# Kernel optimization log

Measured on AMD Instinct MI355X. Metric: run time of the kernel, lower is better.

## Reference

```python
import jax, jax.numpy as jnp
import numpy as np
from functools import partial

MAX_INSTANCES = 8


def _conv(x, W, b):
    y = jax.lax.conv_general_dilated(x, W, (1, 1), 'SAME',
                                     dimension_numbers=('NHWC', 'HWIO', 'NHWC'))
    return jax.nn.relu(y + b)


def _conv_stack(x, params):
    for W, b in params:
        x = _conv(x, W, b)
    return x


def _resize_and_pad(feat, info, bg_h, bg_w):
    # feat: (h, w, c); info: [y1, y2, x1, x2] fractions of bg size.
    # Bilinear resize (half-pixel centers, like tf.image.resize) of feat to
    # (y_size, x_size), then zero-pad into the (bg_h, bg_w) canvas at
    # (y_front, x_front). Expressed as a fixed-shape gather + validity mask
    # so it is jit-compatible despite data-dependent box sizes.
    h, w, _ = feat.shape
    y_size = jnp.maximum((bg_h * (info[1] - info[0])).astype(jnp.int32), 1)
    x_size = jnp.maximum((bg_w * (info[3] - info[2])).astype(jnp.int32), 1)
    y_front = (bg_h * info[0]).astype(jnp.int32)
    x_front = (bg_w * info[2]).astype(jnp.int32)

    def axis(bg_n, front, size, n_in):
        loc = jnp.arange(bg_n) - front
        valid = (loc >= 0) & (loc < size)
        src = (loc.astype(jnp.float32) + 0.5) * (n_in / size.astype(jnp.float32)) - 0.5
        src = jnp.clip(src, 0.0, n_in - 1.0)
        i0 = jnp.floor(src).astype(jnp.int32)
        i1 = jnp.minimum(i0 + 1, n_in - 1)
        return i0, i1, src - i0.astype(jnp.float32), valid

    y0, y1i, fy, vy = axis(bg_h, y_front, y_size, h)
    x0, x1i, fx, vx = axis(bg_w, x_front, x_size, w)
    g = lambda yi, xi: feat[yi][:, xi]  # (bg_h, bg_w, c)
    fy = fy[:, None, None]
    fx = fx[None, :, None]
    out = (g(y0, x0) * (1 - fy) * (1 - fx) + g(y0, x1i) * (1 - fy) * fx
           + g(y1i, x0) * fy * (1 - fx) + g(y1i, x1i) * fy * fx)
    return out * (vy[:, None] & vx[None, :]).astype(feat.dtype)[:, :, None]


def setup_inputs() -> dict:
    key = jax.random.key(0)
    ks = jax.random.split(key, 16)
    B, H, W, C = 4, 128, 128, 64
    h = w = 64
    hm = wm = 56
    U = 64
    MI = MAX_INSTANCES
    instance_feature = jax.random.normal(ks[0], (B, h, w, C, MI), jnp.float32)
    bg_feature = jax.random.normal(ks[1], (B, H, W, C), jnp.float32)
    # Valid boxes: 0 <= y1 < y2 <= 1, 0 <= x1 < x2 <= 1, layout (B, 4, MI).
    y1 = jax.random.uniform(ks[2], (B, 1, MI), minval=0.0, maxval=0.45)
    hh = jax.random.uniform(ks[3], (B, 1, MI), minval=0.2, maxval=0.5)
    x1 = jax.random.uniform(ks[4], (B, 1, MI), minval=0.0, maxval=0.45)
    ww = jax.random.uniform(ks[5], (B, 1, MI), minval=0.2, maxval=0.5)
    bbox = jnp.concatenate([y1, y1 + hh, x1, x1 + ww], axis=1)
    mrcnn_mask = jax.random.uniform(ks[6], (B, hm, wm, MI), jnp.float32)
    s = 0.05  # small weights keep exp() of relu conv outputs well-scaled
    return {
        'instance_feature': instance_feature,
        'bg_feature': bg_feature,
        'bbox': bbox,
        'mrcnn_mask': mrcnn_mask,
        'iW1': jax.random.normal(ks[7], (3, 3, C, U), jnp.float32) * s,
        'ib1': jnp.zeros((U,), jnp.float32),
        'iW2': jax.random.normal(ks[8], (3, 3, U, U), jnp.float32) * s,
        'ib2': jnp.zeros((U,), jnp.float32),
        'iW3': jax.random.normal(ks[9], (3, 3, U, 1), jnp.float32) * s,
        'ib3': jnp.zeros((1,), jnp.float32),
        'bW1': jax.random.normal(ks[10], (3, 3, C, U), jnp.float32) * s,
        'bb1': jnp.zeros((U,), jnp.float32),
        'bW2': jax.random.normal(ks[11], (3, 3, U, U), jnp.float32) * s,
        'bb2': jnp.zeros((U,), jnp.float32),
        'bW3': jax.random.normal(ks[12], (3, 3, U, 1), jnp.float32) * s,
        'bb3': jnp.zeros((1,), jnp.float32),
    }


def reference(instance_feature, bg_feature, bbox, mrcnn_mask,
              iW1, ib1, iW2, ib2, iW3, ib3,
              bW1, bb1, bW2, bb2, bW3, bb3):
    B, H, W, C = bg_feature.shape
    MI = instance_feature.shape[-1]
    h, w = instance_feature.shape[1], instance_feature.shape[2]
    # pack_instance -> conv stack -> unpack (kept as (B, MI, h, w, 1))
    packed = jnp.transpose(instance_feature, (0, 4, 1, 2, 3)).reshape(B * MI, h, w, C)
    iw = _conv_stack(packed, [(iW1, ib1), (iW2, ib2), (iW3, ib3)]).reshape(B, MI, h, w, 1)
    bgw = _conv_stack(bg_feature, [(bW1, bb1), (bW2, bb2), (bW3, bb3)])  # (B,H,W,1)

    rp = jax.vmap(jax.vmap(partial(_resize_and_pad, bg_h=H, bg_w=W)))
    bbox_t = jnp.transpose(bbox, (0, 2, 1))  # (B, MI, 4)
    rw = rp(iw, bbox_t)  # (B, MI, H, W, 1)
    full = jnp.broadcast_to(jnp.array([0.0, 1.0, 0.0, 1.0], jnp.float32), (B, MI, 4))
    rm = rp(jnp.moveaxis(mrcnn_mask, -1, 1)[..., None], full)  # (B, MI, H, W, 1)
    rsf = rp(jnp.moveaxis(instance_feature, -1, 1), bbox_t)  # (B, MI, H, W, C)

    ew = jnp.exp(rw) * rm          # per-instance exp weight, masked
    ew_bg = jnp.exp(bgw)           # (B, H, W, 1)
    denom = ew.sum(axis=1) + ew_bg  # (B, H, W, 1)
    return (ew_bg / denom) * bg_feature + jnp.sum(rsf * (ew / denom[:, None]), axis=1)
```

## Files before the change

### kernel.cpp

```cpp
#include <hip/hip_runtime.h>
#include <cstdint>

typedef short bf16x8 __attribute__((ext_vector_type(8)));
typedef float f32x4 __attribute__((ext_vector_type(4)));
typedef unsigned short u16;
typedef unsigned short u16x8 __attribute__((ext_vector_type(8)));
typedef unsigned int u32;

__device__ inline u16 f2bf(float f) {
  union { float f; unsigned u; } x; x.f = f;
  unsigned u = x.u + 0x7fffu + ((x.u >> 16) & 1u);
  return (u16)(u >> 16);
}
__device__ inline float bf2f(u16 h) {
  union { unsigned u; float f; } x; x.u = ((unsigned)h) << 16;
  return x.f;
}

__global__ __launch_bounds__(256) void transpose_inst(
    const float* __restrict__ inst, u16* __restrict__ pf)
{
  const int lane = threadIdx.x & 63;
  const int wvid = blockIdx.x * 4 + (threadIdx.x >> 6);
  const int b = wvid >> 12;
  const int pix = wvid & 4095;
  const float* s = inst + ((size_t)(b * 4096 + pix)) * 512 + lane * 8;
  float4 v0 = *(const float4*)s;
  float4 v1 = *(const float4*)(s + 4);
  float vals[8] = {v0.x, v0.y, v0.z, v0.w, v1.x, v1.y, v1.z, v1.w};
  #pragma unroll
  for (int i = 0; i < 8; i++)
    pf[(((size_t)(b * 8 + i)) * 4096 + pix) * 64 + lane] = f2bf(vals[i]);
}

__global__ __launch_bounds__(256) void wtrans(
    const float* __restrict__ w0, const float* __restrict__ w1,
    const float* __restrict__ w2, const float* __restrict__ w3,
    u16* __restrict__ wtr)
{
  int id = blockIdx.x * 256 + threadIdx.x;
  if (id >= 147456) return;
  int s = id / 36864;
  int r = id - s * 36864;
  int tap = r >> 12;
  int rc = r & 4095;
  int c = rc >> 6, u = rc & 63;
  const float* Ws = (s == 0) ? w0 : (s == 1) ? w1 : (s == 2) ? w2 : w3;
  wtr[(size_t)s * 36864 + ((size_t)tap * 64 + u) * 64 + c] =
      f2bf(Ws[((size_t)tap * 64 + c) * 64 + u]);
}

#define BOFF 41472
template<int SRC>
__device__ __forceinline__ void conv_body(
    char* smem, const void* __restrict__ inv, const u16* __restrict__ wtr,
    const float* __restrict__ bias, u16* __restrict__ out,
    int H, int W, int bid)
{
  const int tilesX = W >> 4;
  const int tilesPerImg = (H >> 4) * tilesX;
  const int img = bid / tilesPerImg;
  const int tile = bid - img * tilesPerImg;
  const int ty = (tile / tilesX) << 4;
  const int tx = (tile % tilesX) << 4;
  const int tid = threadIdx.x;

  for (int idx = tid; idx < 2592; idx += 256) {
    int hpix = idx >> 3;
    int c0 = (idx & 7) << 3;
    int hy = hpix / 18, hx = hpix - hy * 18;
    int gy = ty + hy - 1, gx = tx + hx - 1;
    u16x8 v = {0, 0, 0, 0, 0, 0, 0, 0};
    if (gy >= 0 && gy < H && gx >= 0 && gx < W) {
      if (SRC == 0) {
        const float* s = (const float*)inv + ((size_t)img * H * W + (size_t)gy * W + gx) * 64 + c0;
        #pragma unroll
        for (int j = 0; j < 8; j++) v[j] = f2bf(s[j]);
      } else if (SRC == 1) {
        const u16* s = (const u16*)inv + ((size_t)img * H * W + (size_t)gy * W + gx) * 64 + c0;
        v = *(const u16x8*)s;
      } else {
        int bb = img >> 3, ii = img & 7;
        const float* s = (const float*)inv + ((((size_t)bb * 64 + gy) * 64 + gx) * 64 + c0) * 8 + ii;
        #pragma unroll
        for (int j = 0; j < 8; j++) v[j] = f2bf(s[j * 8]);
      }
    }
    int byte = (hpix * 128 + c0 * 2) ^ ((hpix & 7) << 4);
    *(u16x8*)(smem + byte) = v;
  }

  const int lane = tid & 63;
  const int wv = tid >> 6;
  const int lrow = lane & 15;
  const int kg = lane >> 4;

  const int ch0 = tid, ch1 = tid + 256;
  const int bu0 = ch0 >> 3, bc0 = (ch0 & 7) << 3;
  const int bu1 = ch1 >> 3, bc1 = (ch1 & 7) << 3;
  const int bdst0 = BOFF + ((bu0 * 128 + bc0 * 2) ^ ((bu0 & 7) << 4));
  const int bdst1 = BOFF + ((bu1 * 128 + bc1 * 2) ^ ((bu1 & 7) << 4));

  {
    u16x8 n0 = *(const u16x8*)(wtr + (size_t)(0 * 64 + bu0) * 64 + bc0);
    u16x8 n1 = *(const u16x8*)(wtr + (size_t)(0 * 64 + bu1) * 64 + bc1);
    *(u16x8*)(smem + bdst0) = n0;
    *(u16x8*)(smem + bdst1) = n1;
  }
  __syncthreads();

  int pyv[4], pxv[4];
  #pragma unroll
  for (int mf = 0; mf < 4; mf++) {
    int p = wv * 64 + mf * 16 + lrow;
    pyv[mf] = p >> 4; pxv[mf] = p & 15;
  }

  f32x4 acc[4][4];
  #pragma unroll
  for (int a = 0; a < 4; a++)
    #pragma unroll
    for (int b = 0; b < 4; b++) { f32x4 z = {0.f, 0.f, 0.f, 0.f}; acc[a][b] = z; }

  for (int tap = 0; tap < 9; tap++) {
    u16x8 n0, n1;
    if (tap < 8) {
      n0 = *(const u16x8*)(wtr + (size_t)((tap + 1) * 64 + bu0) * 64 + bc0);
      n1 = *(const u16x8*)(wtr + (size_t)((tap + 1) * 64 + bu1) * 64 + bc1);
    }
    const int ky = tap / 3, kx = tap - ky * 3;
    #pragma unroll
    for (int ks = 0; ks < 2; ks++) {
      bf16x8 Bf[4];
      #pragma unroll
      for (int nf = 0; nf < 4; nf++) {
        int u = nf * 16 + lrow;
        int byte = BOFF + ((u * 128 + ks * 64 + kg * 16) ^ ((u & 7) << 4));
        Bf[nf] = *(const bf16x8*)(smem + byte);
      }
      #pragma unroll
      for (int mf = 0; mf < 4; mf++) {
        int hpix = (pyv[mf] + ky) * 18 + pxv[mf] + kx;
        int byte = (hpix * 128 + ks * 64 + kg * 16) ^ ((hpix & 7) << 4);
        bf16x8 Af = *(const bf16x8*)(smem + byte);
        #pragma unroll
        for (int nf = 0; nf < 4; nf++)
          acc[mf][nf] = __builtin_amdgcn_mfma_f32_16x16x32_bf16(Af, Bf[nf], acc[mf][nf], 0, 0, 0);
      }
    }
    __syncthreads();
    if (tap < 8) {
      *(u16x8*)(smem + bdst0) = n0;
      *(u16x8*)(smem + bdst1) = n1;
      __syncthreads();
    }
  }

  float bv[4];
  #pragma unroll
  for (int nf = 0; nf < 4; nf++) bv[nf] = bias[nf * 16 + lrow];

  const size_t obase = (size_t)img * H * W;
  #pragma unroll
  for (int mf = 0; mf < 4; mf++) {
    #pragma unroll
    for (int j = 0; j < 4; j++) {
      int p = wv * 64 + mf * 16 + kg * 4 + j;
      int oy = ty + (p >> 4), ox = tx + (p & 15);
      u16* op = out + (obase + (size_t)oy * W + ox) * 64 + lrow;
      #pragma unroll
      for (int nf = 0; nf < 4; nf++)
        op[nf * 16] = f2bf(fmaxf(acc[mf][nf][j] + bv[nf], 0.0f));
    }
  }
}

template<int S1, int S2>
__global__ __launch_bounds__(256) void conv_dual(
    const void* in1, const u16* w1, const float* b1, u16* o1, int H1, int W1, int split,
    const void* in2, const u16* w2, const float* b2, u16* o2, int H2, int W2)
{
  extern __shared__ float4 smem_f4[];
  char* smem = (char*)smem_f4;
  if ((int)blockIdx.x < split)
    conv_body<S1>(smem, in1, w1, b1, o1, H1, W1, blockIdx.x);
  else
    conv_body<S2>(smem, in2, w2, b2, o2, H2, W2, blockIdx.x - split);
}

__device__ __forceinline__ void conv3_body(
    char* smem, const u16* __restrict__ in, const float* __restrict__ W3,
    const float* __restrict__ b3, float* __restrict__ out, int H, int W, int bid)
{
  float* wlds = (float*)(smem + 41472);
  const int tilesX = W >> 4;
  const int tilesPerImg = (H >> 4) * tilesX;
  const int img = bid / tilesPerImg;
  const int tile = bid - img * tilesPerImg;
  const int ty = (tile / tilesX) << 4;
  const int tx = (tile % tilesX) << 4;
  const int tid = threadIdx.x;

  for (int idx = tid; idx < 2592; idx += 256) {
    int hpix = idx >> 3;
    int c0 = (idx & 7) << 3;
    int hy = hpix / 18, hx = hpix - hy * 18;
    int gy = ty + hy - 1, gx = tx + hx - 1;
    u16x8 v = {0, 0, 0, 0, 0, 0, 0, 0};
    if (gy >= 0 && gy < H && gx >= 0 && gx < W)
      v = *(const u16x8*)(in + ((size_t)img * H * W + (size_t)gy * W + gx) * 64 + c0);
    int byte = (hpix * 128 + c0 * 2) ^ ((hpix & 7) << 4);
    *(u16x8*)(smem + byte) = v;
  }
  for (int idx = tid; idx < 576; idx += 256) wlds[idx] = W3[idx];
  __syncthreads();

  const int py = tid >> 4, px = tid & 15;
  float acc = 0.0f;
  #pragma unroll
  for (int ky = 0; ky < 3; ky++) {
    #pragma unroll
    for (int kx = 0; kx < 3; kx++) {
      const int hpix = (py + ky) * 18 + (px + kx);
      const float* wp = wlds + (ky * 3 + kx) * 64;
      #pragma unroll
      for (int cg = 0; cg < 8; cg++) {
        int byte = (hpix * 128 + cg * 16) ^ ((hpix & 7) << 4);
        u16x8 v = *(const u16x8*)(smem + byte);
        #pragma unroll
        for (int j = 0; j < 8; j++)
          acc = fmaf(bf2f(v[j]), wp[cg * 8 + j], acc);
      }
    }
  }
  out[(size_t)img * H * W + (size_t)(ty + py) * W + (tx + px)] =
      fmaxf(acc + b3[0], 0.0f);
}

__global__ __launch_bounds__(256) void conv3_dual(
    const u16* in1, const float* W31, const float* b31, float* o1, int H1, int W1, int split,
    const u16* in2, const float* W32, const float* b32, float* o2, int H2, int W2)
{
  extern __shared__ float4 smem_f4[];
  char* smem = (char*)smem_f4;
  if ((int)blockIdx.x < split)
    conv3_body(smem, in1, W31, b31, o1, H1, W1, blockIdx.x);
  else
    conv3_body(smem, in2, W32, b32, o2, H2, W2, blockIdx.x - split);
}

__global__ __launch_bounds__(256) void precompute_params(
    const float* __restrict__ bbox, const float* __restrict__ mask,
    const float* __restrict__ iw, const float* __restrict__ bgw,
    float* __restrict__ pp_wbg, float* __restrict__ pp_wi,
    u32* __restrict__ pp_yx, float* __restrict__ pp_fy, float* __restrict__ pp_fx)
{
  const int gpix = blockIdx.x * 256 + threadIdx.x;
  const int b = gpix >> 14;
  const int p = gpix & 16383;
  const int Y = p >> 7, X = p & 127;

  float msy = ((float)Y + 0.5f) * 0.4375f - 0.5f;
  msy = fminf(fmaxf(msy, 0.0f), 55.0f);
  int my0 = (int)floorf(msy); int my1 = min(my0 + 1, 55); float fmy = msy - (float)my0;
  float msx = ((float)X + 0.5f) * 0.4375f - 0.5f;
  msx = fminf(fmaxf(msx, 0.0f), 55.0f);
  int mx0 = (int)floorf(msx); int mx1 = min(mx0 + 1, 55); float fmx = msx - (float)mx0;

  const float ewbg = expf(bgw[gpix]);
  float denom = ewbg;
  float wi_l[8];
  u32 yx_l[8];
  float fy_l[8], fx_l[8];

  #pragma unroll
  for (int i = 0; i < 8; i++) {
    float by1 = bbox[(b * 4 + 0) * 8 + i];
    float by2 = bbox[(b * 4 + 1) * 8 + i];
    float bx1 = bbox[(b * 4 + 2) * 8 + i];
    float bx2 = bbox[(b * 4 + 3) * 8 + i];
    int ysz = max((int)(128.0f * (by2 - by1)), 1);
    int xsz = max((int)(128.0f * (bx2 - bx1)), 1);
    int yfr = (int)(128.0f * by1);
    int xfr = (int)(128.0f * bx1);
    int ly = Y - yfr, lx = X - xfr;
    bool valid = (ly >= 0) && (ly < ysz) && (lx >= 0) && (lx < xsz);
    float rwv = 0.0f;
    int y0 = 0, y1i = 0, x0 = 0, x1i = 0;
    float fy = 0.0f, fx = 0.0f;
    if (valid) {
      float sy = ((float)ly + 0.5f) * (64.0f / (float)ysz) - 0.5f;
      sy = fminf(fmaxf(sy, 0.0f), 63.0f);
      y0 = (int)floorf(sy); y1i = min(y0 + 1, 63); fy = sy - (float)y0;
      float sx = ((float)lx + 0.5f) * (64.0f / (float)xsz) - 0.5f;
      sx = fminf(fmaxf(sx, 0.0f), 63.0f);
      x0 = (int)floorf(sx); x1i = min(x0 + 1, 63); fx = sx - (float)x0;
      const float* iwp = iw + ((size_t)(b * 8 + i)) * 4096;
      float v00 = iwp[y0 * 64 + x0],  v01 = iwp[y0 * 64 + x1i];
      float v10 = iwp[y1i * 64 + x0], v11 = iwp[y1i * 64 + x1i];
      rwv = v00 * (1.f - fy) * (1.f - fx) + v01 * (1.f - fy) * fx
          + v10 * fy * (1.f - fx)         + v11 * fy * fx;
    }
    const float* mp = mask + (size_t)b * 56 * 56 * 8 + i;
    float m00 = mp[(my0 * 56 + mx0) * 8], m01 = mp[(my0 * 56 + mx1) * 8];
    float m10 = mp[(my1 * 56 + mx0) * 8], m11 = mp[(my1 * 56 + mx1) * 8];
    float rm = m00 * (1.f - fmy) * (1.f - fmx) + m01 * (1.f - fmy) * fmx
             + m10 * fmy * (1.f - fmx)         + m11 * fmy * fmx;
    float ew = expf(rwv) * rm;
    denom += ew;
    wi_l[i] = valid ? ew : 0.0f;
    yx_l[i] = (u32)y0 | ((u32)x0 << 8) | ((u32)y1i << 16) | ((u32)x1i << 24);
    fy_l[i] = fy; fx_l[i] = fx;
  }

  const float invd = 1.0f / denom;
  pp_wbg[gpix] = ewbg * invd;
  #pragma unroll
  for (int i = 0; i < 8; i++) {
    pp_wi[i * 65536 + gpix] = wi_l[i] * invd;
    pp_yx[i * 65536 + gpix] = yx_l[i];
    pp_fy[i * 65536 + gpix] = fy_l[i];
    pp_fx[i * 65536 + gpix] = fx_l[i];
  }
}

__global__ __launch_bounds__(256) void final_blend(
    const u16* __restrict__ pf, const float* __restrict__ bgf,
    const float* __restrict__ pp_wbg, const float* __restrict__ pp_wi,
    const u32* __restrict__ pp_yx, const float* __restrict__ pp_fy,
    const float* __restrict__ pp_fx, float* __restrict__ out)
{
  const int lane = threadIdx.x & 63;
  const int gpix = blockIdx.x * 4 + (threadIdx.x >> 6);
  const int b = gpix >> 14;

  float accv = pp_wbg[gpix] * bgf[(size_t)gpix * 64 + lane];
  #pragma unroll
  for (int i = 0; i < 8; i++) {
    float wiv = pp_wi[i * 65536 + gpix];
    if (wiv != 0.0f) {
      u32 yx = pp_yx[i * 65536 + gpix];
      float fy = pp_fy[i * 65536 + gpix];
      float fx = pp_fx[i * 65536 + gpix];
      int y0 = yx & 255, x0 = (yx >> 8) & 255;
      int y1i = (yx >> 16) & 255, x1i = (yx >> 24) & 255;
      const u16* fp = pf + (size_t)(b * 8 + i) * 262144;
      float g00 = bf2f(fp[((size_t)(y0 * 64 + x0)) * 64 + lane]);
      float g01 = bf2f(fp[((size_t)(y0 * 64 + x1i)) * 64 + lane]);
      float g10 = bf2f(fp[((size_t)(y1i * 64 + x0)) * 64 + lane]);
      float g11 = bf2f(fp[((size_t)(y1i * 64 + x1i)) * 64 + lane]);
      float s = g00 * (1.f - fy) * (1.f - fx) + g01 * (1.f - fy) * fx
              + g10 * fy * (1.f - fx)         + g11 * fy * fx;
      accv = fmaf(wiv, s, accv);
    }
  }
  out[(size_t)gpix * 64 + lane] = accv;
}

__global__ __launch_bounds__(256) void final_kernel_fb(
    const float* __restrict__ inst, const float* __restrict__ bgf,
    const float* __restrict__ bbox, const float* __restrict__ mask,
    const float* __restrict__ iw, const float* __restrict__ bgw,
    float* __restrict__ out)
{
  const int lane = threadIdx.x & 63;
  const int wvid = blockIdx.x * 4 + (threadIdx.x >> 6);
  const int nw = gridDim.x * 4;
  for (int pix = wvid; pix < 4 * 128 * 128; pix += nw) {
    const int b = pix >> 14;
    const int p = pix & 16383;
    const int Y = p >> 7, X = p & 127;

    float msy = ((float)Y + 0.5f) * 0.4375f - 0.5f;
    msy = fminf(fmaxf(msy, 0.0f), 55.0f);
    int my0 = (int)floorf(msy); int my1 = min(my0 + 1, 55); float fmy = msy - (float)my0;
    float msx = ((float)X + 0.5f) * 0.4375f - 0.5f;
    msx = fminf(fmaxf(msx, 0.0f), 55.0f);
    int mx0 = (int)floorf(msx); int mx1 = min(mx0 + 1, 55); float fmx = msx - (float)mx0;

    const float ewbg = expf(bgw[(size_t)b * 16384 + p]);
    float denom = ewbg;
    float acc = 0.0f;

    for (int i = 0; i < 8; i++) {
      float by1 = bbox[(b * 4 + 0) * 8 + i];
      float by2 = bbox[(b * 4 + 1) * 8 + i];
      float bx1 = bbox[(b * 4 + 2) * 8 + i];
      float bx2 = bbox[(b * 4 + 3) * 8 + i];
      int ysz = max((int)(128.0f * (by2 - by1)), 1);
      int xsz = max((int)(128.0f * (bx2 - bx1)), 1);
      int yfr = (int)(128.0f * by1);
      int xfr = (int)(128.0f * bx1);
      int ly = Y - yfr, lx = X - xfr;
      bool valid = (ly >= 0) && (ly < ysz) && (lx >= 0) && (lx < xsz);
      float rwv = 0.0f;
      int y0 = 0, y1i = 0, x0 = 0, x1i = 0;
      float fy = 0.0f, fx = 0.0f;
      if (valid) {
        float sy = ((float)ly + 0.5f) * (64.0f / (float)ysz) - 0.5f;
        sy = fminf(fmaxf(sy, 0.0f), 63.0f);
        y0 = (int)floorf(sy); y1i = min(y0 + 1, 63); fy = sy - (float)y0;
        float sx = ((float)lx + 0.5f) * (64.0f / (float)xsz) - 0.5f;
        sx = fminf(fmaxf(sx, 0.0f), 63.0f);
        x0 = (int)floorf(sx); x1i = min(x0 + 1, 63); fx = sx - (float)x0;
        const float* iwp = iw + ((size_t)(b * 8 + i)) * 4096;
        float v00 = iwp[y0 * 64 + x0],  v01 = iwp[y0 * 64 + x1i];
        float v10 = iwp[y1i * 64 + x0], v11 = iwp[y1i * 64 + x1i];
        rwv = v00 * (1.f - fy) * (1.f - fx) + v01 * (1.f - fy) * fx
            + v10 * fy * (1.f - fx)         + v11 * fy * fx;
      }
      const float* mp = mask + (size_t)b * 56 * 56 * 8 + i;
      float m00 = mp[(my0 * 56 + mx0) * 8], m01 = mp[(my0 * 56 + mx1) * 8];
      float m10 = mp[(my1 * 56 + mx0) * 8], m11 = mp[(my1 * 56 + mx1) * 8];
      float rm = m00 * (1.f - fmy) * (1.f - fmx) + m01 * (1.f - fmy) * fmx
               + m10 * fmy * (1.f - fmx)         + m11 * fmy * fmx;
      float ew = expf(rwv) * rm;
      denom += ew;
      if (valid) {
        const float* fp = inst + (size_t)b * 2097152 + i;
        float g00 = fp[(((size_t)y0 * 64 + x0) * 64 + lane) * 8];
        float g01 = fp[(((size_t)y0 * 64 + x1i) * 64 + lane) * 8];
        float g10 = fp[(((size_t)y1i * 64 + x0) * 64 + lane) * 8];
        float g11 = fp[(((size_t)y1i * 64 + x1i) * 64 + lane) * 8];
        float s = g00 * (1.f - fy) * (1.f - fx) + g01 * (1.f - fy) * fx
                + g10 * fy * (1.f - fx)         + g11 * fy * fx;
        acc += ew * s;
      }
    }
    const float bgv = bgf[((size_t)b * 16384 + p) * 64 + lane];
    out[((size_t)b * 16384 + p) * 64 + lane] = (ewbg * bgv + acc) / denom;
  }
}

extern "C" void kernel_launch(void* const* d_in, const int* in_sizes, int n_in,
                              void* d_out, int out_size, void* d_ws, size_t ws_size,
                              hipStream_t stream) {
  const float* inst = (const float*)d_in[0];
  const float* bgf  = (const float*)d_in[1];
  const float* bbox = (const float*)d_in[2];
  const float* mask = (const float*)d_in[3];
  const float* iW1 = (const float*)d_in[4];  const float* ib1 = (const float*)d_in[5];
  const float* iW2 = (const float*)d_in[6];  const float* ib2 = (const float*)d_in[7];
  const float* iW3 = (const float*)d_in[8];  const float* ib3 = (const float*)d_in[9];
  const float* bW1 = (const float*)d_in[10]; const float* bb1 = (const float*)d_in[11];
  const float* bW2 = (const float*)d_in[12]; const float* bb2 = (const float*)d_in[13];
  const float* bW3 = (const float*)d_in[14]; const float* bb3 = (const float*)d_in[15];

  char* ws = (char*)d_ws;
  u16*   wtr  = (u16*)ws;
  u16*   AbI  = (u16*)(ws + 294912);
  u16*   AbB  = (u16*)(ws + 17072128);
  u16*   BbI  = (u16*)(ws + 25460736);
  u16*   BbB  = (u16*)(ws + 42237952);
  float* iw   = (float*)(ws + 50626560);
  float* bgw  = (float*)(ws + 51150848);
  u16*   pf   = (u16*)(ws + 51412992);
  const bool usePf = ws_size >= (size_t)68190208;
  float* outp = (float*)d_out;

  float* pp_wbg = (float*)(ws + 294912);
  float* pp_wi  = (float*)(ws + 294912 + 262144);
  u32*   pp_yx  = (u32*)  (ws + 294912 + 2359296);
  float* pp_fy  = (float*)(ws + 294912 + 4456448);
  float* pp_fx  = (float*)(ws + 294912 + 6553600);

  wtrans<<<576, 256, 0, stream>>>(iW1, iW2, bW1, bW2, wtr);

  if (usePf) {
    transpose_inst<<<4096, 256, 0, stream>>>(inst, pf);
    conv_dual<1, 0><<<768, 256, 49664, stream>>>(
        pf,  wtr,             ib1, AbI, 64, 64, 512,
        bgf, wtr + 2 * 36864, bb1, AbB, 128, 128);
    conv_dual<1, 1><<<768, 256, 49664, stream>>>(
        AbI, wtr + 36864,     ib2, BbI, 64, 64, 512,
        AbB, wtr + 3 * 36864, bb2, BbB, 128, 128);
    conv3_dual<<<768, 256, 43776, stream>>>(
        BbI, iW3, ib3, iw, 64, 64, 512,
        BbB, bW3, bb3, bgw, 128, 128);
    precompute_params<<<256, 256, 0, stream>>>(bbox, mask, iw, bgw,
        pp_wbg, pp_wi, pp_yx, pp_fy, pp_fx);
    final_blend<<<16384, 256, 0, stream>>>(pf, bgf,
        pp_wbg, pp_wi, pp_yx, pp_fy, pp_fx, outp);
  } else {
    conv_dual<2, 0><<<768, 256, 49664, stream>>>(
        inst, wtr,            ib1, AbI, 64, 64, 512,
        bgf, wtr + 2 * 36864, bb1, AbB, 128, 128);
    conv_dual<1, 1><<<768, 256, 49664, stream>>>(
        AbI, wtr + 36864,     ib2, BbI, 64, 64, 512,
        AbB, wtr + 3 * 36864, bb2, BbB, 128, 128);
    conv3_dual<<<768, 256, 43776, stream>>>(
        BbI, iW3, ib3, iw, 64, 64, 512,
        BbB, bW3, bb3, bgw, 128, 128);
    final_kernel_fb<<<2048, 256, 0, stream>>>(inst, bgf, bbox, mask, iw, bgw, outp);
  }
}
```

Measured before the change: 130.1 us.

## Load conv weight fragments from global into registers and merge prep kernels

Weight fragments for each conv tap are now read straight from global memory into registers and double-buffered across taps. This replaces staging them through LDS, which needed two block barriers per tap. The LDS footprint shrinks by the weight buffer, which may let more blocks fit per CU. The weight transpose and the instance transpose are fused into one prep kernel to save a launch. In exchange, every wave issues its own global loads for the weights and holds extra VGPRs for the B buffers, and the fallback path now also writes pf even when the workspace may be too small for it.

```diff
diff --git a/kernel.cpp b/kernel.cpp
--- a/kernel.cpp
+++ b/kernel.cpp
@@ -17,40 +17,38 @@
   return x.f;
 }
 
-__global__ __launch_bounds__(256) void transpose_inst(
-    const float* __restrict__ inst, u16* __restrict__ pf)
-{
-  const int lane = threadIdx.x & 63;
-  const int wvid = blockIdx.x * 4 + (threadIdx.x >> 6);
-  const int b = wvid >> 12;
-  const int pix = wvid & 4095;
-  const float* s = inst + ((size_t)(b * 4096 + pix)) * 512 + lane * 8;
-  float4 v0 = *(const float4*)s;
-  float4 v1 = *(const float4*)(s + 4);
-  float vals[8] = {v0.x, v0.y, v0.z, v0.w, v1.x, v1.y, v1.z, v1.w};
-  #pragma unroll
-  for (int i = 0; i < 8; i++)
-    pf[(((size_t)(b * 8 + i)) * 4096 + pix) * 64 + lane] = f2bf(vals[i]);
-}
-
-__global__ __launch_bounds__(256) void wtrans(
+__global__ __launch_bounds__(256) void prep_kernel(
+    const float* __restrict__ inst, u16* __restrict__ pf,
     const float* __restrict__ w0, const float* __restrict__ w1,
     const float* __restrict__ w2, const float* __restrict__ w3,
     u16* __restrict__ wtr)
 {
-  int id = blockIdx.x * 256 + threadIdx.x;
-  if (id >= 147456) return;
-  int s = id / 36864;
-  int r = id - s * 36864;
-  int tap = r >> 12;
-  int rc = r & 4095;
-  int c = rc >> 6, u = rc & 63;
-  const float* Ws = (s == 0) ? w0 : (s == 1) ? w1 : (s == 2) ? w2 : w3;
-  wtr[(size_t)s * 36864 + ((size_t)tap * 64 + u) * 64 + c] =
-      f2bf(Ws[((size_t)tap * 64 + c) * 64 + u]);
-}
-
-#define BOFF 41472
+  if (blockIdx.x < 4096) {
+    const int lane = threadIdx.x & 63;
+    const int wvid = blockIdx.x * 4 + (threadIdx.x >> 6);
+    const int b = wvid >> 12;
+    const int pix = wvid & 4095;
+    const float* s = inst + ((size_t)(b * 4096 + pix)) * 512 + lane * 8;
+    float4 v0 = *(const float4*)s;
+    float4 v1 = *(const float4*)(s + 4);
+    float vals[8] = {v0.x, v0.y, v0.z, v0.w, v1.x, v1.y, v1.z, v1.w};
+    #pragma unroll
+    for (int i = 0; i < 8; i++)
+      pf[(((size_t)(b * 8 + i)) * 4096 + pix) * 64 + lane] = f2bf(vals[i]);
+  } else {
+    int id = (blockIdx.x - 4096) * 256 + threadIdx.x;
+    if (id >= 147456) return;
+    int s = id / 36864;
+    int r = id - s * 36864;
+    int tap = r >> 12;
+    int rc = r & 4095;
+    int c = rc >> 6, u = rc & 63;
+    const float* Ws = (s == 0) ? w0 : (s == 1) ? w1 : (s == 2) ? w2 : w3;
+    wtr[(size_t)s * 36864 + ((size_t)tap * 64 + u) * 64 + c] =
+        f2bf(Ws[((size_t)tap * 64 + c) * 64 + u]);
+  }
+}
+
 template<int SRC>
 __device__ __forceinline__ void conv_body(
     char* smem, const void* __restrict__ inv, const u16* __restrict__ wtr,
@@ -95,19 +93,7 @@
   const int lrow = lane & 15;
   const int kg = lane >> 4;
 
-  const int ch0 = tid, ch1 = tid + 256;
-  const int bu0 = ch0 >> 3, bc0 = (ch0 & 7) << 3;
-  const int bu1 = ch1 >> 3, bc1 = (ch1 & 7) << 3;
-  const int bdst0 = BOFF + ((bu0 * 128 + bc0 * 2) ^ ((bu0 & 7) << 4));
-  const int bdst1 = BOFF + ((bu1 * 128 + bc1 * 2) ^ ((bu1 & 7) << 4));
-
-  {
-    u16x8 n0 = *(const u16x8*)(wtr + (size_t)(0 * 64 + bu0) * 64 + bc0);
-    u16x8 n1 = *(const u16x8*)(wtr + (size_t)(0 * 64 + bu1) * 64 + bc1);
-    *(u16x8*)(smem + bdst0) = n0;
-    *(u16x8*)(smem + bdst1) = n1;
-  }
-  __syncthreads();
+  const u16* bfrag = wtr + (size_t)lrow * 64 + kg * 8;
 
   int pyv[4], pxv[4];
   #pragma unroll
@@ -122,22 +108,27 @@
     #pragma unroll
     for (int b = 0; b < 4; b++) { f32x4 z = {0.f, 0.f, 0.f, 0.f}; acc[a][b] = z; }
 
+  bf16x8 Bcur[2][4], Bnext[2][4];
+  #pragma unroll
+  for (int ks = 0; ks < 2; ks++)
+    #pragma unroll
+    for (int nf = 0; nf < 4; nf++)
+      Bcur[ks][nf] = *(const bf16x8*)(bfrag + nf * 1024 + ks * 32);
+
+  __syncthreads();
+
   for (int tap = 0; tap < 9; tap++) {
-    u16x8 n0, n1;
     if (tap < 8) {
-      n0 = *(const u16x8*)(wtr + (size_t)((tap + 1) * 64 + bu0) * 64 + bc0);
-      n1 = *(const u16x8*)(wtr + (size_t)((tap + 1) * 64 + bu1) * 64 + bc1);
+      const u16* bn = bfrag + (size_t)(tap + 1) * 4096;
+      #pragma unroll
+      for (int ks = 0; ks < 2; ks++)
+        #pragma unroll
+        for (int nf = 0; nf < 4; nf++)
+          Bnext[ks][nf] = *(const bf16x8*)(bn + nf * 1024 + ks * 32);
     }
     const int ky = tap / 3, kx = tap - ky * 3;
     #pragma unroll
     for (int ks = 0; ks < 2; ks++) {
-      bf16x8 Bf[4];
-      #pragma unroll
-      for (int nf = 0; nf < 4; nf++) {
-        int u = nf * 16 + lrow;
-        int byte = BOFF + ((u * 128 + ks * 64 + kg * 16) ^ ((u & 7) << 4));
-        Bf[nf] = *(const bf16x8*)(smem + byte);
-      }
       #pragma unroll
       for (int mf = 0; mf < 4; mf++) {
         int hpix = (pyv[mf] + ky) * 18 + pxv[mf] + kx;
@@ -145,15 +136,14 @@
         bf16x8 Af = *(const bf16x8*)(smem + byte);
         #pragma unroll
         for (int nf = 0; nf < 4; nf++)
-          acc[mf][nf] = __builtin_amdgcn_mfma_f32_16x16x32_bf16(Af, Bf[nf], acc[mf][nf], 0, 0, 0);
+          acc[mf][nf] = __builtin_amdgcn_mfma_f32_16x16x32_bf16(Af, Bcur[ks][nf], acc[mf][nf], 0, 0, 0);
       }
     }
-    __syncthreads();
-    if (tap < 8) {
-      *(u16x8*)(smem + bdst0) = n0;
-      *(u16x8*)(smem + bdst1) = n1;
-      __syncthreads();
-    }
+    #pragma unroll
+    for (int ks = 0; ks < 2; ks++)
+      #pragma unroll
+      for (int nf = 0; nf < 4; nf++)
+        Bcur[ks][nf] = Bnext[ks][nf];
   }
 
   float bv[4];
@@ -464,14 +454,12 @@
   float* pp_fy  = (float*)(ws + 294912 + 4456448);
   float* pp_fx  = (float*)(ws + 294912 + 6553600);
 
-  wtrans<<<576, 256, 0, stream>>>(iW1, iW2, bW1, bW2, wtr);
-
   if (usePf) {
-    transpose_inst<<<4096, 256, 0, stream>>>(inst, pf);
-    conv_dual<1, 0><<<768, 256, 49664, stream>>>(
+    prep_kernel<<<4672, 256, 0, stream>>>(inst, pf, iW1, iW2, bW1, bW2, wtr);
+    conv_dual<1, 0><<<768, 256, 41472, stream>>>(
         pf,  wtr,             ib1, AbI, 64, 64, 512,
         bgf, wtr + 2 * 36864, bb1, AbB, 128, 128);
-    conv_dual<1, 1><<<768, 256, 49664, stream>>>(
+    conv_dual<1, 1><<<768, 256, 41472, stream>>>(
         AbI, wtr + 36864,     ib2, BbI, 64, 64, 512,
         AbB, wtr + 3 * 36864, bb2, BbB, 128, 128);
     conv3_dual<<<768, 256, 43776, stream>>>(
@@ -482,10 +470,11 @@
     final_blend<<<16384, 256, 0, stream>>>(pf, bgf,
         pp_wbg, pp_wi, pp_yx, pp_fy, pp_fx, outp);
   } else {
-    conv_dual<2, 0><<<768, 256, 49664, stream>>>(
+    prep_kernel<<<4672, 256, 0, stream>>>(inst, pf, iW1, iW2, bW1, bW2, wtr);
+    conv_dual<2, 0><<<768, 256, 41472, stream>>>(
         inst, wtr,            ib1, AbI, 64, 64, 512,
         bgf, wtr + 2 * 36864, bb1, AbB, 128, 128);
-    conv_dual<1, 1><<<768, 256, 49664, stream>>>(
+    conv_dual<1, 1><<<768, 256, 41472, stream>>>(
         AbI, wtr + 36864,     ib2, BbI, 64, 64, 512,
         AbB, wtr + 3 * 36864, bb2, BbB, 128, 128);
     conv3_dual<<<768, 256, 43776, stream>>>(
```

Result: slower. 166.9 us (+28.3%).
